# Kernel optimization log

Measured on AMD Instinct MI355X. Metric: run time of the kernel, lower is better.

The kernel has to match this reference:

```python
import jax, jax.numpy as jnp
import numpy as np

B, D, H, HD, L = 2, 768, 16, 48, 3
N_IMG, N_PAST, T_DEC = 1024, 16, 20

def _ln(x, g, b, eps=1e-5):
    m = jnp.mean(x, axis=-1, keepdims=True)
    v = jnp.mean(jnp.square(x - m), axis=-1, keepdims=True)
    return (x - m) * jax.lax.rsqrt(v + eps) * g + b

def _encoder(x, ln1_g, ln1_b, qkv_W, qkv_b, out_W, out_b, ln2_g, ln2_b, ff1_W, ff1_b, ff2_W, ff2_b):
    Bs, S, _ = x.shape
    keep = jnp.tril(jnp.ones((S, S), dtype=bool))  # causal: True = attend
    neg = jnp.asarray(jnp.finfo(x.dtype).min, x.dtype)
    scale = 1.0 / np.sqrt(HD)
    for l in range(L):  # pre-norm TransformerEncoderLayer, activation=relu (torch default)
        h = _ln(x, ln1_g[l], ln1_b[l])
        q, k, v = jnp.split(h @ qkv_W[l] + qkv_b[l], 3, axis=-1)
        q = q.reshape(Bs, S, H, HD); k = k.reshape(Bs, S, H, HD); v = v.reshape(Bs, S, H, HD)
        scores = jnp.einsum('bqhd,bkhd->bhqk', q, k) * scale
        attn = jax.nn.softmax(jnp.where(keep, scores, neg), axis=-1)
        ctx = jnp.einsum('bhqk,bkhd->bqhd', attn, v).reshape(Bs, S, H * HD)
        x = x + ctx @ out_W[l] + out_b[l]
        h = _ln(x, ln2_g[l], ln2_b[l])
        x = x + jax.nn.relu(h @ ff1_W[l] + ff1_b[l]) @ ff2_W[l] + ff2_b[l]
    return x

def setup_inputs():
    key = jax.random.key(0)
    ks = jax.random.split(key, 16)
    rn = lambda i, shp, s=0.02: jax.random.normal(ks[i], shp, jnp.float32) * s
    return {
        'feats': jax.random.normal(ks[0], (B, D, N_IMG), jnp.float32),
        'past': jax.random.normal(ks[1], (B, N_PAST, 6), jnp.float32),
        'intent': jax.random.randint(ks[2], (B,), 0, 3),
        'img_pos_enc': rn(3, (1, N_IMG, D)),
        'time_embeds': rn(4, (36, D)),
        'intent_embeds': rn(5, (3, D)),
        'past_W': rn(6, (6, D)), 'past_b': jnp.zeros((D,), jnp.float32),
        'pos_W': rn(7, (2, D)), 'pos_b': jnp.zeros((D,), jnp.float32),
        'ln1_g': jnp.ones((L, D), jnp.float32), 'ln1_b': jnp.zeros((L, D), jnp.float32),
        'qkv_W': rn(8, (L, D, 3 * D)), 'qkv_b': jnp.zeros((L, 3 * D), jnp.float32),
        'out_W': rn(9, (L, D, D)), 'out_b': jnp.zeros((L, D), jnp.float32),
        'ln2_g': jnp.ones((L, D), jnp.float32), 'ln2_b': jnp.zeros((L, D), jnp.float32),
        'ff1_W': rn(10, (L, D, 4 * D)), 'ff1_b': jnp.zeros((L, 4 * D), jnp.float32),
        'ff2_W': rn(11, (L, 4 * D, D)), 'ff2_b': jnp.zeros((L, D), jnp.float32),
        'dec1_W': rn(12, (D, D)), 'dec1_b': jnp.zeros((D,), jnp.float32),
        'dec2_W': rn(13, (D, 2)), 'dec2_b': jnp.zeros((2,), jnp.float32),
    }

def reference(feats, past, intent, img_pos_enc, time_embeds, intent_embeds,
              past_W, past_b, pos_W, pos_b,
              ln1_g, ln1_b, qkv_W, qkv_b, out_W, out_b, ln2_g, ln2_b,
              ff1_W, ff1_b, ff2_W, ff2_b, dec1_W, dec1_b, dec2_W, dec2_b):
    # context: 1024 image tokens + 1 intent token + 16 past tokens
    img_tokens = jnp.transpose(feats, (0, 2, 1)) + img_pos_enc          # [B, 1024, D]
    intent_idx = jnp.clip(intent - 1, 0, 2)
    intent_tok = intent_embeds[intent_idx][:, None, :]                  # [B, 1, D]
    past_toks = past @ past_W + past_b + time_embeds[:N_PAST]           # [B, 16, D]
    seq = jnp.concatenate([img_tokens, intent_tok, past_toks], axis=1)  # [B, 1041, D]
    enc = lambda s: _encoder(s, ln1_g, ln1_b, qkv_W, qkv_b, out_W, out_b,
                             ln2_g, ln2_b, ff1_W, ff1_b, ff2_W, ff2_b)
    preds = []
    for t in range(T_DEC):  # AR decode: full recompute each step, no KV cache (as in source)
        out = enc(seq)
        h = out[:, -1:, :]
        p = jax.nn.gelu(h @ dec1_W + dec1_b, approximate=False) @ dec2_W + dec2_b  # [B,1,2]
        preds.append(p)
        nxt = p @ pos_W + pos_b + time_embeds[N_PAST + t]
        seq = jnp.concatenate([seq, nxt], axis=1)
    return jnp.concatenate(preds, axis=1)  # [B, 20, 2]
```

## Files before the change

### kernel.cpp

```cpp
#include <hip/hip_runtime.h>
#include <math.h>

#define BB 2
#define DD 768
#define HH 16
#define HDIM 48
#define LL 3
#define NIMG 1024
#define NPAST 16
#define TDEC 20
#define SEQ0 1041
#define SPAD 1064
#define MM (BB*SEQ0)
#define SCALE_QK 0.14433756729740643f
#define KVL_C ((size_t)BB*HH*SPAD*HDIM)

typedef __attribute__((ext_vector_type(4))) float f32x4;
typedef __attribute__((ext_vector_type(8))) short bf16x8;

__device__ __forceinline__ short f2bf(float x) {
  unsigned u = __float_as_uint(x);
  unsigned r = (u + 0x7FFFu + ((u >> 16) & 1u)) >> 16;
  return (short)r;
}
__device__ __forceinline__ float bf2f(short h) {
  return __uint_as_float(((unsigned)(unsigned short)h) << 16);
}

__device__ __forceinline__ float block_sum256(float v, float* red) {
#pragma unroll
  for (int off = 32; off; off >>= 1) v += __shfl_down(v, off);
  __syncthreads();
  if ((threadIdx.x & 63) == 0) red[threadIdx.x >> 6] = v;
  __syncthreads();
  return red[0] + red[1] + red[2] + red[3];
}

__global__ __launch_bounds__(256) void build_img_kernel(
    const float* __restrict__ feats, const float* __restrict__ pe, float* __restrict__ x)
{
  __shared__ float T[64][65];
  int b = blockIdx.y;
  int s0 = blockIdx.x * 64;
  int tid = threadIdx.x;
  int r = tid >> 2;
  int c0 = (tid & 3) << 4;
  for (int d0 = 0; d0 < 768; d0 += 64) {
    const float* fp = feats + ((size_t)b*768 + d0 + r)*1024 + s0 + c0;
#pragma unroll
    for (int i = 0; i < 16; ++i) T[r][c0 + i] = fp[i];
    __syncthreads();
    float* xp = x + ((size_t)(b*SEQ0 + s0 + r))*768 + d0 + c0;
    const float* pp = pe + (size_t)(s0 + r)*768 + d0 + c0;
#pragma unroll
    for (int i = 0; i < 16; ++i) xp[i] = T[c0 + i][r] + pp[i];
    __syncthreads();
  }
}

__global__ __launch_bounds__(256) void build_misc_kernel(
    const float* __restrict__ past, const int* __restrict__ intent,
    const float* __restrict__ int_emb, const float* __restrict__ past_W,
    const float* __restrict__ past_b, const float* __restrict__ te,
    float* __restrict__ x)
{
  int b = blockIdx.y;
  int i = blockIdx.x;
  int tid = threadIdx.x;
  if (i == 0) {
    int idx = intent[b] - 1;
    idx = max(0, min(2, idx));
    for (int d = tid; d < 768; d += 256)
      x[((size_t)(b*SEQ0 + 1024))*768 + d] = int_emb[idx*768 + d];
  } else {
    int pi = i - 1;
    float p0 = past[(b*NPAST + pi)*6 + 0], p1 = past[(b*NPAST + pi)*6 + 1];
    float p2 = past[(b*NPAST + pi)*6 + 2], p3 = past[(b*NPAST + pi)*6 + 3];
    float p4 = past[(b*NPAST + pi)*6 + 4], p5 = past[(b*NPAST + pi)*6 + 5];
    for (int d = tid; d < 768; d += 256) {
      float s = past_b[d] + te[(size_t)pi*768 + d];
      s += p0*past_W[0*768 + d] + p1*past_W[1*768 + d] + p2*past_W[2*768 + d];
      s += p3*past_W[3*768 + d] + p4*past_W[4*768 + d] + p5*past_W[5*768 + d];
      x[((size_t)(b*SEQ0 + 1025 + pi))*768 + d] = s;
    }
  }
}

__global__ __launch_bounds__(256) void ln_kernel(
    const float* __restrict__ x, const float* __restrict__ g,
    const float* __restrict__ bta, float* __restrict__ h)
{
  __shared__ float red[4];
  size_t row = blockIdx.x;
  const float* xr = x + row*768;
  float* hr = h + row*768;
  int tid = threadIdx.x;
  float v0 = xr[tid], v1 = xr[tid+256], v2 = xr[tid+512];
  float m = block_sum256(v0+v1+v2, red) * (1.f/768.f);
  float d0 = v0-m, d1 = v1-m, d2 = v2-m;
  float var = block_sum256(d0*d0 + d1*d1 + d2*d2, red) * (1.f/768.f);
  float inv = rsqrtf(var + 1e-5f);
  hr[tid]     = d0*inv*g[tid]     + bta[tid];
  hr[tid+256] = d1*inv*g[tid+256] + bta[tid+256];
  hr[tid+512] = d2*inv*g[tid+512] + bta[tid+512];
}

__global__ __launch_bounds__(256) void wconv_kernel(
    const float* __restrict__ W, short* __restrict__ th, short* __restrict__ tl,
    int K, int N)
{
  __shared__ float T[64][68];
  int n0 = blockIdx.x * 64, k0 = blockIdx.y * 64;
  int t = threadIdx.x;
  int r = t >> 2, c0 = (t & 3) * 16;
  const float* src = W + (size_t)(k0 + r)*N + n0 + c0;
#pragma unroll
  for (int j = 0; j < 4; ++j) {
    f32x4 v = *(const f32x4*)(src + 4*j);
    T[r][c0 + 4*j + 0] = v.x; T[r][c0 + 4*j + 1] = v.y;
    T[r][c0 + 4*j + 2] = v.z; T[r][c0 + 4*j + 3] = v.w;
  }
  __syncthreads();
  bf16x8 h0, h1, l0, l1;
#pragma unroll
  for (int i = 0; i < 8; ++i) {
    float x = T[c0 + i][r];
    short hh = f2bf(x);
    h0[i] = hh; l0[i] = f2bf(x - bf2f(hh));
    float y = T[c0 + 8 + i][r];
    short hy = f2bf(y);
    h1[i] = hy; l1[i] = f2bf(y - bf2f(hy));
  }
  size_t dst = (size_t)(n0 + r)*K + k0 + c0;
  *(bf16x8*)(th + dst) = h0;
  *(bf16x8*)(th + dst + 8) = h1;
  *(bf16x8*)(tl + dst) = l0;
  *(bf16x8*)(tl + dst + 8) = l1;
}

__global__ __launch_bounds__(256) void gemm_mfma_kernel(
    const float* __restrict__ A, const short* __restrict__ Wh,
    const short* __restrict__ Wl, const float* __restrict__ bias,
    float* __restrict__ C, int M, int N, int K, int mode)
{
  __shared__ short As[2][128][40];
  __shared__ short Bs[2][128][40];
  int tid = threadIdx.x;
  int n0 = blockIdx.x * 128, m0 = blockIdx.y * 128;
  int wid = tid >> 6, l = tid & 63;
  int wm = wid >> 1, wn = wid & 1;
  int fr = l & 15, fk = (l >> 4) * 8;
  f32x4 acc[4][4] = {};
  int arow = tid >> 1, akh = (tid & 1) * 16;
  const float* aptr = A + (size_t)(m0 + arow)*K + akh;
  bool aval = (m0 + arow) < M;

  for (int k0 = 0; k0 < K; k0 += 32) {
    {
      float xv[16];
      if (aval) {
        const float* ap = aptr + k0;
#pragma unroll
        for (int j = 0; j < 4; ++j) {
          f32x4 v = *(const f32x4*)(ap + 4*j);
          xv[4*j+0] = v.x; xv[4*j+1] = v.y; xv[4*j+2] = v.z; xv[4*j+3] = v.w;
        }
      } else {
#pragma unroll
        for (int j = 0; j < 16; ++j) xv[j] = 0.f;
      }
      bf16x8 h0, h1, l0, l1;
#pragma unroll
      for (int e = 0; e < 8; ++e) {
        short hh = f2bf(xv[e]);
        h0[e] = hh; l0[e] = f2bf(xv[e] - bf2f(hh));
        short hy = f2bf(xv[8+e]);
        h1[e] = hy; l1[e] = f2bf(xv[8+e] - bf2f(hy));
      }
      *(bf16x8*)&As[0][arow][akh]     = h0;
      *(bf16x8*)&As[0][arow][akh + 8] = h1;
      *(bf16x8*)&As[1][arow][akh]     = l0;
      *(bf16x8*)&As[1][arow][akh + 8] = l1;
    }
#pragma unroll
    for (int cc = 0; cc < 2; ++cc) {
      int c = tid + cc*256;
      int row = c >> 2, woff = (c & 3) * 8;
      size_t src = (size_t)(n0 + row)*K + k0 + woff;
      *(bf16x8*)&Bs[0][row][woff] = *(const bf16x8*)(Wh + src);
      *(bf16x8*)&Bs[1][row][woff] = *(const bf16x8*)(Wl + src);
    }
    __syncthreads();
    bf16x8 af[4][2], bfv[4][2];
#pragma unroll
    for (int i = 0; i < 4; ++i) {
#pragma unroll
      for (int p = 0; p < 2; ++p) {
        af[i][p]  = *(const bf16x8*)&As[p][wm*64 + i*16 + fr][fk];
        bfv[i][p] = *(const bf16x8*)&Bs[p][wn*64 + i*16 + fr][fk];
      }
    }
#pragma unroll
    for (int im = 0; im < 4; ++im) {
#pragma unroll
      for (int in = 0; in < 4; ++in) {
        acc[im][in] = __builtin_amdgcn_mfma_f32_16x16x32_bf16(af[im][0], bfv[in][0], acc[im][in], 0, 0, 0);
        acc[im][in] = __builtin_amdgcn_mfma_f32_16x16x32_bf16(af[im][0], bfv[in][1], acc[im][in], 0, 0, 0);
        acc[im][in] = __builtin_amdgcn_mfma_f32_16x16x32_bf16(af[im][1], bfv[in][0], acc[im][in], 0, 0, 0);
      }
    }
    __syncthreads();
  }
#pragma unroll
  for (int in = 0; in < 4; ++in) {
    int n = n0 + wn*64 + in*16 + (l & 15);
    float bv = bias[n];
#pragma unroll
    for (int im = 0; im < 4; ++im) {
      f32x4 v = acc[im][in];
#pragma unroll
      for (int r = 0; r < 4; ++r) {
        int m = m0 + wm*64 + im*16 + (l >> 4)*4 + r;
        if (m < M) {
          float x = v[r] + bv;
          float* cp = &C[(size_t)m*N + n];
          if (mode == 1) x = fmaxf(x, 0.f);
          if (mode == 2) x += *cp;
          *cp = x;
        }
      }
    }
  }
}

__global__ __launch_bounds__(256) void scatter_kv_kernel(
    const float* __restrict__ qkv, float* __restrict__ kc, float* __restrict__ vc,
    int S, int spad)
{
  int s = blockIdx.x, b = blockIdx.y;
  const float* row = qkv + ((size_t)b*S + s)*2304;
  int tid = threadIdx.x;
#pragma unroll
  for (int i = 0; i < 3; ++i) {
    int j = tid + i*256;
    int hh = j / 48, hd = j - hh*48;
    size_t dst = ((size_t)(b*16 + hh)*spad + s)*48 + hd;
    kc[dst] = row[768 + j];
    vc[dst] = row[1536 + j];
  }
}

__global__ __launch_bounds__(256) void attn_prefill_kernel(
    const float* __restrict__ qkv, const float* __restrict__ Kc,
    const float* __restrict__ Vc, float* __restrict__ ctx, int S, int spad)
{
  __shared__ float Qs[32][49];
  __shared__ float Ks[64][49];
  __shared__ float Vs[64][49];
  __shared__ float Ps[32][65];
  __shared__ float mrow[32], lrow[32], resc[32];
  int tid = threadIdx.x;
  int qt = blockIdx.x, h = blockIdx.y, b = blockIdx.z;
  int q0 = qt * 32;
  for (int i = tid; i < 32*48; i += 256) {
    int r = i / 48, d = i - r*48;
    int s = q0 + r;
    Qs[r][d] = (s < S) ? qkv[((size_t)(b*S + s))*2304 + h*48 + d] * SCALE_QK : 0.f;
  }
  if (tid < 32) { mrow[tid] = -INFINITY; lrow[tid] = 0.f; }
  float acc[2][3] = {};
  int pr0 = (tid >> 4) << 1;
  int pc  = tid & 15;
  int sr  = tid & 31;
  int skg = tid >> 5;
  int q_last = min(q0 + 31, S - 1);
  const float* Kb = Kc + (size_t)(b*16 + h)*spad*48;
  const float* Vb = Vc + (size_t)(b*16 + h)*spad*48;
  __syncthreads();
  float qreg[48];
#pragma unroll
  for (int d = 0; d < 48; ++d) qreg[d] = Qs[sr][d];
  for (int k0 = 0; k0 <= q_last; k0 += 64) {
    int kn = min(64, q_last - k0 + 1);
    for (int i = tid; i < 64*48; i += 256) {
      int r = i / 48, d = i - r*48;
      bool ok = r < kn;
      Ks[r][d] = ok ? Kb[(size_t)(k0 + r)*48 + d] : 0.f;
      Vs[r][d] = ok ? Vb[(size_t)(k0 + r)*48 + d] : 0.f;
    }
    __syncthreads();
    {
      int qg = q0 + sr;
#pragma unroll
      for (int jj = 0; jj < 8; ++jj) {
        int k = skg*8 + jj;
        float s = 0.f;
#pragma unroll
        for (int d = 0; d < 48; ++d) s += qreg[d] * Ks[k][d];
        int kg = k0 + k;
        bool valid = (qg < S) && (k < kn) && (kg <= qg);
        Ps[sr][k] = valid ? s : -INFINITY;
      }
    }
    __syncthreads();
    {
      int r = tid >> 3;
      int c0 = (tid & 7) * 8;
      float mold = mrow[r];
      float mx = mold;
      float pv[8];
#pragma unroll
      for (int j = 0; j < 8; ++j) { pv[j] = Ps[r][c0 + j]; mx = fmaxf(mx, pv[j]); }
#pragma unroll
      for (int m = 1; m < 8; m <<= 1) mx = fmaxf(mx, __shfl_xor(mx, m));
      float psum = 0.f;
      if (mx > -INFINITY) {
#pragma unroll
        for (int j = 0; j < 8; ++j) {
          float p = __expf(pv[j] - mx);
          Ps[r][c0 + j] = p;
          psum += p;
        }
      } else {
#pragma unroll
        for (int j = 0; j < 8; ++j) Ps[r][c0 + j] = 0.f;
      }
#pragma unroll
      for (int m = 1; m < 8; m <<= 1) psum += __shfl_xor(psum, m);
      if ((tid & 7) == 0) {
        if (mx > -INFINITY) {
          float rs = (mold > -INFINITY) ? __expf(mold - mx) : 0.f;
          lrow[r] = lrow[r]*rs + psum;
          mrow[r] = mx;
          resc[r] = rs;
        } else {
          resc[r] = 1.f;
        }
      }
    }
    __syncthreads();
#pragma unroll
    for (int rr = 0; rr < 2; ++rr) {
      int r = pr0 + rr;
      float f = resc[r];
      float a0 = acc[rr][0]*f, a1 = acc[rr][1]*f, a2 = acc[rr][2]*f;
#pragma unroll 16
      for (int k = 0; k < 64; ++k) {
        float p = Ps[r][k];
        a0 += p * Vs[k][pc*3+0];
        a1 += p * Vs[k][pc*3+1];
        a2 += p * Vs[k][pc*3+2];
      }
      acc[rr][0] = a0; acc[rr][1] = a1; acc[rr][2] = a2;
    }
    __syncthreads();
  }
#pragma unroll
  for (int rr = 0; rr < 2; ++rr) {
    int r = pr0 + rr, s = q0 + r;
    if (s < S) {
      float invl = 1.f / lrow[r];
      float* cp = &ctx[((size_t)(b*S + s))*768 + h*48 + pc*3];
      cp[0] = acc[rr][0]*invl; cp[1] = acc[rr][1]*invl; cp[2] = acc[rr][2]*invl;
    }
  }
}

struct DecParams {
  const float *qkv_W, *qkv_b, *out_W, *out_b;
  const float *ln1_g, *ln1_b, *ln2_g, *ln2_b;
  const float *ff1_W, *ff1_b, *ff2_W, *ff2_b;
  const float *dec1_W, *dec1_b, *dec2_W, *dec2_b;
  const float *pos_W, *pos_b, *time_e;
  const float *xlast;
  float *Kc, *Vc;
  float *x_tok, *x_in_buf, *x_mid_buf;
  float *qkv_part, *out_part, *ff1_part, *ff2_part, *dec1_part;
  float *attn_m, *attn_l, *attn_o;
  float *outp;
};

__global__ __launch_bounds__(256) void k_qkvA(DecParams P, int l) {
  int p = blockIdx.x;
  __shared__ float xin[2][768];
  __shared__ float hn[2][768];
  __shared__ float part[4][2][64];
  __shared__ float red[4];
  int tid = threadIdx.x;
  if (l == 0) {
    for (int i = tid; i < 1536; i += 256) ((float*)xin)[i] = P.x_tok[i];
  } else {
    for (int i = tid; i < 1536; i += 256) {
      float v = P.x_mid_buf[i];
#pragma unroll
      for (int s = 0; s < 21; ++s) v += P.ff2_part[s*1536 + i];
      ((float*)xin)[i] = v;
    }
  }
  __syncthreads();
  if (p == 0) {
    for (int i = tid; i < 1536; i += 256) P.x_in_buf[i] = ((float*)xin)[i];
  }
  const float* g  = P.ln1_g + l*768;
  const float* be = P.ln1_b + l*768;
#pragma unroll
  for (int b = 0; b < 2; ++b) {
    float v0 = xin[b][tid], v1 = xin[b][tid+256], v2 = xin[b][tid+512];
    float m = block_sum256(v0+v1+v2, red) * (1.f/768.f);
    float d0=v0-m, d1=v1-m, d2=v2-m;
    float var = block_sum256(d0*d0+d1*d1+d2*d2, red) * (1.f/768.f);
    float inv = rsqrtf(var + 1e-5f);
    hn[b][tid]     = d0*inv*g[tid]     + be[tid];
    hn[b][tid+256] = d1*inv*g[tid+256] + be[tid+256];
    hn[b][tid+512] = d2*inv*g[tid+512] + be[tid+512];
  }
  __syncthreads();
  int nt = p % 36, ks = p / 36;
  int k0 = (ks*768)/7, k1 = ((ks+1)*768)/7;
  int w = tid >> 6, lane = tid & 63;
  int kw0 = k0 + ((k1-k0)*w)/4, kw1 = k0 + ((k1-k0)*(w+1))/4;
  int n = nt*64 + lane;
  const float* wp = P.qkv_W + (size_t)l*768*2304 + n;
  float a0 = 0.f, a1 = 0.f;
#pragma unroll 4
  for (int k = kw0; k < kw1; ++k) {
    float w_ = wp[(size_t)k*2304];
    a0 += hn[0][k]*w_; a1 += hn[1][k]*w_;
  }
  part[w][0][lane] = a0; part[w][1][lane] = a1;
  __syncthreads();
  if (tid < 128) {
    int b = tid>>6, ln = tid&63;
    float s = part[0][b][ln]+part[1][b][ln]+part[2][b][ln]+part[3][b][ln];
    P.qkv_part[ks*4608 + b*2304 + nt*64 + ln] = s;
  }
}

__global__ __launch_bounds__(256) void k_attn(DecParams P, int l, int pos) {
  __shared__ float qs[48], ksn[48], vsn[48];
  __shared__ float redm[4], reds[4];
  __shared__ float aw[4][48];
  int p = blockIdx.x;
  int b = p >> 7, h = (p >> 3) & 15, s = p & 7;
  int tid = threadIdx.x;
  const float* qb = P.qkv_b + l*2304;
  if (tid < 48) {
    float q  = qb[h*48+tid];
    float kk = qb[768 + h*48+tid];
    float vv = qb[1536 + h*48+tid];
#pragma unroll
    for (int ss = 0; ss < 7; ++ss) {
      const float* pp = P.qkv_part + ss*4608 + b*2304;
      q  += pp[h*48+tid];
      kk += pp[768 + h*48+tid];
      vv += pp[1536 + h*48+tid];
    }
    if (s == 7) {
      size_t coff = (size_t)l*KVL_C + ((size_t)(b*16+h)*SPAD + pos)*48 + tid;
      P.Kc[coff] = kk;
      P.Vc[coff] = vv;
    }
    qs[tid] = q * SCALE_QK; ksn[tid] = kk; vsn[tid] = vv;
  }
  __syncthreads();
  int CH = (pos + 7) >> 3;
  int r0 = s*CH, r1 = min(r0 + CH, pos);
  int nold = r1 - r0;
  bool is_new = (s == 7) && (tid == nold);
  bool active = (tid < nold) || is_new;
  const float* Kb = P.Kc + (size_t)l*KVL_C + (size_t)(b*16+h)*SPAD*48;
  const float* Vb = P.Vc + (size_t)l*KVL_C + (size_t)(b*16+h)*SPAD*48;
  float sc = -INFINITY;
  if (tid < nold) {
    const float4* kr = (const float4*)(Kb + (size_t)(r0+tid)*48);
    float ssum = 0.f;
#pragma unroll
    for (int i = 0; i < 12; ++i) {
      float4 kv = kr[i];
      ssum += qs[4*i]*kv.x + qs[4*i+1]*kv.y + qs[4*i+2]*kv.z + qs[4*i+3]*kv.w;
    }
    sc = ssum;
  } else if (is_new) {
    float ssum = 0.f;
#pragma unroll
    for (int d = 0; d < 48; ++d) ssum += qs[d]*ksn[d];
    sc = ssum;
  }
  float mx = sc;
#pragma unroll
  for (int o2 = 32; o2; o2 >>= 1) mx = fmaxf(mx, __shfl_down(mx, o2));
  if ((tid & 63) == 0) redm[tid >> 6] = mx;
  __syncthreads();
  float M = fmaxf(fmaxf(redm[0], redm[1]), fmaxf(redm[2], redm[3]));
  float pr = active ? __expf(sc - M) : 0.f;
  float lsum = block_sum256(pr, reds);
  float4 a[12];
  if (tid < nold) {
    const float4* vr = (const float4*)(Vb + (size_t)(r0+tid)*48);
#pragma unroll
    for (int i = 0; i < 12; ++i) {
      float4 vv = vr[i];
      a[i].x = pr*vv.x; a[i].y = pr*vv.y; a[i].z = pr*vv.z; a[i].w = pr*vv.w;
    }
  } else if (is_new) {
#pragma unroll
    for (int i = 0; i < 12; ++i) {
      a[i].x = pr*vsn[4*i]; a[i].y = pr*vsn[4*i+1];
      a[i].z = pr*vsn[4*i+2]; a[i].w = pr*vsn[4*i+3];
    }
  } else {
#pragma unroll
    for (int i = 0; i < 12; ++i) a[i] = make_float4(0.f,0.f,0.f,0.f);
  }
#pragma unroll
  for (int i = 0; i < 12; ++i) {
    float x0=a[i].x, x1=a[i].y, x2=a[i].z, x3=a[i].w;
#pragma unroll
    for (int o2 = 32; o2; o2 >>= 1) {
      x0 += __shfl_down(x0, o2); x1 += __shfl_down(x1, o2);
      x2 += __shfl_down(x2, o2); x3 += __shfl_down(x3, o2);
    }
    if ((tid & 63) == 0) {
      int w = tid >> 6;
      aw[w][4*i] = x0; aw[w][4*i+1] = x1; aw[w][4*i+2] = x2; aw[w][4*i+3] = x3;
    }
  }
  __syncthreads();
  int idx = (b*16 + h)*8 + s;
  if (tid == 0) { P.attn_m[idx] = M; P.attn_l[idx] = lsum; }
  if (tid < 48) P.attn_o[idx*48 + tid] = aw[0][tid]+aw[1][tid]+aw[2][tid]+aw[3][tid];
}

__global__ __launch_bounds__(256) void k_out(DecParams P, int l) {
  int p = blockIdx.x;
  __shared__ float ctx_s[2][96];
  __shared__ float opart[4][2][64][2];
  int nt = p / 8, ks = p % 8;
  int k0 = ks * 96;
  int tid = threadIdx.x;
  if (tid < 192) {
    int b = tid / 96, dl = tid % 96;
    int d = k0 + dl;
    int h = d / 48, dd = d % 48;
    int base = (b*16 + h)*8;
    float M = -INFINITY;
#pragma unroll
    for (int s2 = 0; s2 < 8; ++s2) M = fmaxf(M, P.attn_m[base+s2]);
    float L = 0.f, o = 0.f;
#pragma unroll
    for (int s2 = 0; s2 < 8; ++s2) {
      float e = __expf(P.attn_m[base+s2] - M);
      L += P.attn_l[base+s2]*e;
      o += P.attn_o[(base+s2)*48 + dd]*e;
    }
    ctx_s[b][dl] = o / L;
  }
  __syncthreads();
  int w = tid >> 6, lane = tid & 63;
  int n0 = nt * 128;
  const float* W = P.out_W + (size_t)l*768*768;
  float a00=0.f, a01=0.f, a10=0.f, a11=0.f;
#pragma unroll 4
  for (int j = w*24; j < w*24 + 24; ++j) {
    int kk = k0 + j;
    float2 wv = *(const float2*)&W[(size_t)kk*768 + n0 + lane*2];
    float c0 = ctx_s[0][j], c1 = ctx_s[1][j];
    a00 += c0*wv.x; a01 += c0*wv.y;
    a10 += c1*wv.x; a11 += c1*wv.y;
  }
  opart[w][0][lane][0] = a00; opart[w][0][lane][1] = a01;
  opart[w][1][lane][0] = a10; opart[w][1][lane][1] = a11;
  __syncthreads();
  {
    int b = tid >> 7, idx = tid & 127;
    int l2 = idx >> 1, c = idx & 1;
    float v = opart[0][b][l2][c] + opart[1][b][l2][c]
            + opart[2][b][l2][c] + opart[3][b][l2][c];
    P.out_part[ks*1536 + b*768 + n0 + idx] = v;
  }
}

__global__ __launch_bounds__(256) void k_ff1A(DecParams P, int l) {
  int p = blockIdx.x;
  __shared__ float xm[2][768];
  __shared__ float hn[2][768];
  __shared__ float part[4][2][64];
  __shared__ float red[4];
  int tid = threadIdx.x;
  const float* ob = P.out_b + l*768;
  for (int i = tid; i < 1536; i += 256) {
    int b = i / 768, d = i - b*768;
    float v = P.x_in_buf[i] + ob[d];
#pragma unroll
    for (int s = 0; s < 8; ++s) v += P.out_part[s*1536 + i];
    xm[b][d] = v;
  }
  __syncthreads();
  if (p == 0) {
    for (int i = tid; i < 1536; i += 256) P.x_mid_buf[i] = ((float*)xm)[i];
  }
  const float* g  = P.ln2_g + l*768;
  const float* be = P.ln2_b + l*768;
#pragma unroll
  for (int b = 0; b < 2; ++b) {
    float v0 = xm[b][tid], v1 = xm[b][tid+256], v2 = xm[b][tid+512];
    float m = block_sum256(v0+v1+v2, red) * (1.f/768.f);
    float d0=v0-m, d1=v1-m, d2=v2-m;
    float var = block_sum256(d0*d0+d1*d1+d2*d2, red) * (1.f/768.f);
    float inv = rsqrtf(var + 1e-5f);
    hn[b][tid]     = d0*inv*g[tid]     + be[tid];
    hn[b][tid+256] = d1*inv*g[tid+256] + be[tid+256];
    hn[b][tid+512] = d2*inv*g[tid+512] + be[tid+512];
  }
  __syncthreads();
  int nt = p % 48, ks = p / 48;
  int k0 = (ks*768)/5, k1 = ((ks+1)*768)/5;
  int w = tid >> 6, lane = tid & 63;
  int kw0 = k0 + ((k1-k0)*w)/4, kw1 = k0 + ((k1-k0)*(w+1))/4;
  int n = nt*64 + lane;
  const float* wp = P.ff1_W + (size_t)l*768*3072 + n;
  float a0 = 0.f, a1 = 0.f;
#pragma unroll 4
  for (int k = kw0; k < kw1; ++k) {
    float w_ = wp[(size_t)k*3072];
    a0 += hn[0][k]*w_; a1 += hn[1][k]*w_;
  }
  part[w][0][lane] = a0; part[w][1][lane] = a1;
  __syncthreads();
  if (tid < 128) {
    int b = tid>>6, ln = tid&63;
    float s = part[0][b][ln]+part[1][b][ln]+part[2][b][ln]+part[3][b][ln];
    P.ff1_part[ks*6144 + b*3072 + nt*64 + ln] = s;
  }
}

__global__ __launch_bounds__(256) void k_ff2A(DecParams P, int l) {
  int p = blockIdx.x;
  __shared__ float hseg[2][148];
  __shared__ float part[4][2][64];
  int tid = threadIdx.x;
  int nt = p % 12, ks = p / 12;
  int k0 = (ks*3072)/21, k1 = ((ks+1)*3072)/21;
  int kn = k1 - k0;
  const float* fb = P.ff1_b + l*3072;
  for (int i = tid; i < 2*kn; i += 256) {
    int b = i / kn, j = i - b*kn;
    float v = fb[k0+j];
#pragma unroll
    for (int s = 0; s < 5; ++s) v += P.ff1_part[s*6144 + b*3072 + k0 + j];
    hseg[b][j] = fmaxf(v, 0.f);
  }
  __syncthreads();
  int w = tid >> 6, lane = tid & 63;
  int jw0 = (kn*w)/4, jw1 = (kn*(w+1))/4;
  int n = nt*64 + lane;
  const float* wp = P.ff2_W + (size_t)l*3072*768 + n;
  float a0 = 0.f, a1 = 0.f;
#pragma unroll 4
  for (int j = jw0; j < jw1; ++j) {
    float w_ = wp[(size_t)(k0+j)*768];
    a0 += hseg[0][j]*w_; a1 += hseg[1][j]*w_;
  }
  part[w][0][lane] = a0; part[w][1][lane] = a1;
  __syncthreads();
  if (tid < 128) {
    int b = tid>>6, ln = tid&63;
    P.ff2_part[ks*1536 + b*768 + nt*64 + ln] =
        part[0][b][ln]+part[1][b][ln]+part[2][b][ln]+part[3][b][ln];
  }
}

__global__ __launch_bounds__(256) void k_dec1A(DecParams P, int t) {
  int p = blockIdx.x;
  __shared__ float hseg[2][40];
  __shared__ float part[4][2][64];
  int tid = threadIdx.x;
  int nt = p % 12, ks = p / 12;
  int k0 = (ks*768)/21, k1 = ((ks+1)*768)/21;
  int kn = k1 - k0;
  for (int i = tid; i < 2*kn; i += 256) {
    int b = i / kn, j = i - b*kn;
    float v;
    if (t == 0) {
      v = P.xlast[(size_t)b*SEQ0*768 + k0 + j];
    } else {
      v = P.x_mid_buf[b*768 + k0 + j];
#pragma unroll
      for (int s = 0; s < 21; ++s) v += P.ff2_part[s*1536 + b*768 + k0 + j];
    }
    hseg[b][j] = v;
  }
  __syncthreads();
  int w = tid >> 6, lane = tid & 63;
  int jw0 = (kn*w)/4, jw1 = (kn*(w+1))/4;
  int n = nt*64 + lane;
  const float* wp = P.dec1_W + n;
  float a0 = 0.f, a1 = 0.f;
#pragma unroll 4
  for (int j = jw0; j < jw1; ++j) {
    float w_ = wp[(size_t)(k0+j)*768];
    a0 += hseg[0][j]*w_; a1 += hseg[1][j]*w_;
  }
  part[w][0][lane] = a0; part[w][1][lane] = a1;
  __syncthreads();
  if (tid < 128) {
    int b = tid>>6, ln = tid&63;
    P.dec1_part[ks*1536 + b*768 + nt*64 + ln] =
        part[0][b][ln]+part[1][b][ln]+part[2][b][ln]+part[3][b][ln];
  }
}

__global__ __launch_bounds__(256) void k_head2(DecParams P, int t, int write_next) {
  __shared__ float hd[2][768];
  __shared__ float ps[2][2];
  int tid = threadIdx.x;
  for (int i = tid; i < 1536; i += 256) {
    int b = i / 768, d = i - b*768;
    float v = P.dec1_b[d];
#pragma unroll
    for (int s = 0; s < 21; ++s) v += P.dec1_part[s*1536 + i];
    hd[b][d] = 0.5f*v*(1.f + erff(v*0.70710678118654752f));
  }
  __syncthreads();
  int w = tid >> 6, lane = tid & 63;
  int b = w >> 1, j = w & 1;
  float partial = 0.f;
  for (int k = lane; k < 768; k += 64) partial += hd[b][k] * P.dec2_W[k*2 + j];
#pragma unroll
  for (int off = 32; off; off >>= 1) partial += __shfl_down(partial, off);
  if (lane == 0) {
    float v = partial + P.dec2_b[j];
    ps[b][j] = v;
    P.outp[(b*TDEC + t)*2 + j] = v;
  }
  __syncthreads();
  if (write_next) {
    for (int i = tid; i < 1536; i += 256) {
      int b2 = i / 768, d = i - b2*768;
      P.x_tok[i] = ps[b2][0]*P.pos_W[d] + ps[b2][1]*P.pos_W[768 + d]
                 + P.pos_b[d] + P.time_e[(size_t)(NPAST + t)*768 + d];
    }
  }
}

extern "C" void kernel_launch(void* const* d_in, const int* in_sizes, int n_in,
                              void* d_out, int out_size, void* d_ws, size_t ws_size,
                              hipStream_t stream) {
  (void)in_sizes; (void)n_in; (void)out_size; (void)ws_size;
  const float* feats   = (const float*)d_in[0];
  const float* past    = (const float*)d_in[1];
  const int*   intent  = (const int*)d_in[2];
  const float* img_pos = (const float*)d_in[3];
  const float* time_e  = (const float*)d_in[4];
  const float* int_emb = (const float*)d_in[5];
  const float* past_W  = (const float*)d_in[6];
  const float* past_b  = (const float*)d_in[7];
  const float* pos_W   = (const float*)d_in[8];
  const float* pos_b   = (const float*)d_in[9];
  const float* ln1_g   = (const float*)d_in[10];
  const float* ln1_b   = (const float*)d_in[11];
  const float* qkv_W   = (const float*)d_in[12];
  const float* qkv_b   = (const float*)d_in[13];
  const float* out_W   = (const float*)d_in[14];
  const float* out_b   = (const float*)d_in[15];
  const float* ln2_g   = (const float*)d_in[16];
  const float* ln2_b   = (const float*)d_in[17];
  const float* ff1_W   = (const float*)d_in[18];
  const float* ff1_b   = (const float*)d_in[19];
  const float* ff2_W   = (const float*)d_in[20];
  const float* ff2_b   = (const float*)d_in[21];
  const float* dec1_W  = (const float*)d_in[22];
  const float* dec1_b  = (const float*)d_in[23];
  const float* dec2_W  = (const float*)d_in[24];
  const float* dec2_b  = (const float*)d_in[25];
  float* outp = (float*)d_out;

  float* ws = (float*)d_ws;
  size_t off = 0;
  float* xbuf = ws + off;   off += (size_t)MM*DD;
  float* hbuf = ws + off;   off += (size_t)MM*DD;
  float* ctxbuf = hbuf;
  float* bigbuf = ws + off; off += (size_t)MM*3072;
  float* Kc = ws + off;     off += (size_t)LL*BB*HH*SPAD*HDIM;
  float* Vc = ws + off;     off += (size_t)LL*BB*HH*SPAD*HDIM;
  float* x_tok = ws + off;    off += BB*DD;
  float* x_in_buf = ws + off; off += BB*DD;
  float* x_mid_buf = ws + off; off += BB*DD;
  float* qkv_part = ws + off;  off += 7*2*2304;
  float* out_part = ws + off;  off += 8*2*768;
  float* ff1_part = ws + off;  off += 5*2*3072;
  float* ff2_part = ws + off;  off += 21*2*768;
  float* dec1_part = ws + off; off += 21*2*768;
  float* attn_m = ws + off;    off += 2*16*8;
  float* attn_l = ws + off;    off += 2*16*8;
  float* attn_o = ws + off;    off += 2*16*8*48;
  short* wt_h = (short*)(ws + off); off += (size_t)768*3072/2;
  short* wt_l = (short*)(ws + off); off += (size_t)768*3072/2;

  const size_t KVL = (size_t)BB*HH*SPAD*HDIM;

  build_img_kernel<<<dim3(NIMG/64, BB), 256, 0, stream>>>(feats, img_pos, xbuf);
  build_misc_kernel<<<dim3(17, BB), 256, 0, stream>>>(past, intent, int_emb, past_W, past_b, time_e, xbuf);

  const int mtiles = (MM + 127) / 128;
  for (int l = 0; l < LL; ++l) {
    float* kcl = Kc + (size_t)l*KVL;
    float* vcl = Vc + (size_t)l*KVL;

    ln_kernel<<<MM, 256, 0, stream>>>(xbuf, ln1_g + l*DD, ln1_b + l*DD, hbuf);
    wconv_kernel<<<dim3(2304/64, 768/64), 256, 0, stream>>>(
        qkv_W + (size_t)l*DD*2304, wt_h, wt_l, DD, 2304);
    gemm_mfma_kernel<<<dim3(2304/128, mtiles), 256, 0, stream>>>(
        hbuf, wt_h, wt_l, qkv_b + l*2304, bigbuf, MM, 2304, DD, 0);

    scatter_kv_kernel<<<dim3(SEQ0, BB), 256, 0, stream>>>(bigbuf, kcl, vcl, SEQ0, SPAD);
    attn_prefill_kernel<<<dim3((SEQ0 + 31)/32, HH, BB), 256, 0, stream>>>(
        bigbuf, kcl, vcl, ctxbuf, SEQ0, SPAD);

    wconv_kernel<<<dim3(768/64, 768/64), 256, 0, stream>>>(
        out_W + (size_t)l*DD*DD, wt_h, wt_l, DD, 768);
    gemm_mfma_kernel<<<dim3(768/128, mtiles), 256, 0, stream>>>(
        ctxbuf, wt_h, wt_l, out_b + l*DD, xbuf, MM, 768, DD, 2);

    ln_kernel<<<MM, 256, 0, stream>>>(xbuf, ln2_g + l*DD, ln2_b + l*DD, hbuf);
    wconv_kernel<<<dim3(3072/64, 768/64), 256, 0, stream>>>(
        ff1_W + (size_t)l*DD*3072, wt_h, wt_l, DD, 3072);
    gemm_mfma_kernel<<<dim3(3072/128, mtiles), 256, 0, stream>>>(
        hbuf, wt_h, wt_l, ff1_b + l*3072, bigbuf, MM, 3072, DD, 1);

    wconv_kernel<<<dim3(768/64, 3072/64), 256, 0, stream>>>(
        ff2_W + (size_t)l*3072*DD, wt_h, wt_l, 3072, 768);
    gemm_mfma_kernel<<<dim3(768/128, mtiles), 256, 0, stream>>>(
        bigbuf, wt_h, wt_l, ff2_b + l*DD, xbuf, MM, 768, 3072, 2);
  }

  DecParams P;
  P.qkv_W = qkv_W; P.qkv_b = qkv_b; P.out_W = out_W; P.out_b = out_b;
  P.ln1_g = ln1_g; P.ln1_b = ln1_b; P.ln2_g = ln2_g; P.ln2_b = ln2_b;
  P.ff1_W = ff1_W; P.ff1_b = ff1_b; P.ff2_W = ff2_W; P.ff2_b = ff2_b;
  P.dec1_W = dec1_W; P.dec1_b = dec1_b; P.dec2_W = dec2_W; P.dec2_b = dec2_b;
  P.pos_W = pos_W; P.pos_b = pos_b; P.time_e = time_e;
  P.xlast = xbuf + (size_t)(SEQ0 - 1)*DD;
  P.Kc = Kc; P.Vc = Vc;
  P.x_tok = x_tok; P.x_in_buf = x_in_buf; P.x_mid_buf = x_mid_buf;
  P.qkv_part = qkv_part; P.out_part = out_part; P.ff1_part = ff1_part;
  P.ff2_part = ff2_part; P.dec1_part = dec1_part;
  P.attn_m = attn_m; P.attn_l = attn_l; P.attn_o = attn_o;
  P.outp = outp;

  k_dec1A<<<252, 256, 0, stream>>>(P, 0);
  k_head2<<<1, 256, 0, stream>>>(P, 0, 1);
  for (int t = 1; t < TDEC; ++t) {
    int pos = SEQ0 + t - 1;
    for (int l = 0; l < LL; ++l) {
      k_qkvA<<<252, 256, 0, stream>>>(P, l);
      k_attn<<<256, 256, 0, stream>>>(P, l, pos);
      k_out<<<48, 256, 0, stream>>>(P, l);
      k_ff1A<<<240, 256, 0, stream>>>(P, l);
      k_ff2A<<<252, 256, 0, stream>>>(P, l);
    }
    k_dec1A<<<252, 256, 0, stream>>>(P, t);
    k_head2<<<1, 256, 0, stream>>>(P, t, (t < TDEC - 1) ? 1 : 0);
  }
}
```

Measured before the change: 4.975 ms.

## Emit split-bf16 activations from producers and fuse KV scatter into QKV GEMM

Producer kernels (layernorm, attention output, FF1 GEMM epilogue) now write activations directly as hi/lo bf16 pairs, so the GEMM loads bf16 tiles instead of converting fp32 inputs every k-step. The standalone scatter_kv kernel is removed and the QKV GEMM epilogue writes K and V straight into the cache layout. This cuts redundant conversion work (each A tile was re-split once per N-tile block) and one kernel launch with its memory pass. The cost is scattered, uncoalesced stores in the QKV epilogue.

```diff
diff --git a/kernel.cpp b/kernel.cpp
--- a/kernel.cpp
+++ b/kernel.cpp
@@ -86,23 +86,27 @@
   }
 }
 
-__global__ __launch_bounds__(256) void ln_kernel(
+__global__ __launch_bounds__(256) void ln_bf_kernel(
     const float* __restrict__ x, const float* __restrict__ g,
-    const float* __restrict__ bta, float* __restrict__ h)
+    const float* __restrict__ bta, short* __restrict__ hh, short* __restrict__ hl)
 {
   __shared__ float red[4];
   size_t row = blockIdx.x;
   const float* xr = x + row*768;
-  float* hr = h + row*768;
   int tid = threadIdx.x;
   float v0 = xr[tid], v1 = xr[tid+256], v2 = xr[tid+512];
   float m = block_sum256(v0+v1+v2, red) * (1.f/768.f);
   float d0 = v0-m, d1 = v1-m, d2 = v2-m;
   float var = block_sum256(d0*d0 + d1*d1 + d2*d2, red) * (1.f/768.f);
   float inv = rsqrtf(var + 1e-5f);
-  hr[tid]     = d0*inv*g[tid]     + bta[tid];
-  hr[tid+256] = d1*inv*g[tid+256] + bta[tid+256];
-  hr[tid+512] = d2*inv*g[tid+512] + bta[tid+512];
+  float o0 = d0*inv*g[tid]     + bta[tid];
+  float o1 = d1*inv*g[tid+256] + bta[tid+256];
+  float o2 = d2*inv*g[tid+512] + bta[tid+512];
+  short h0 = f2bf(o0), h1 = f2bf(o1), h2 = f2bf(o2);
+  size_t base = row*768;
+  hh[base+tid]     = h0; hl[base+tid]     = f2bf(o0 - bf2f(h0));
+  hh[base+tid+256] = h1; hl[base+tid+256] = f2bf(o1 - bf2f(h1));
+  hh[base+tid+512] = h2; hl[base+tid+512] = f2bf(o2 - bf2f(h2));
 }
 
 __global__ __launch_bounds__(256) void wconv_kernel(
@@ -138,10 +142,13 @@
   *(bf16x8*)(tl + dst + 8) = l1;
 }
 
-__global__ __launch_bounds__(256) void gemm_mfma_kernel(
-    const float* __restrict__ A, const short* __restrict__ Wh,
-    const short* __restrict__ Wl, const float* __restrict__ bias,
-    float* __restrict__ C, int M, int N, int K, int mode)
+__global__ __launch_bounds__(256) void gemm_bf_kernel(
+    const short* __restrict__ Ah, const short* __restrict__ Al,
+    const short* __restrict__ Wh, const short* __restrict__ Wl,
+    const float* __restrict__ bias, float* __restrict__ C,
+    short* __restrict__ Ch, short* __restrict__ Cl,
+    int M, int N, int K, int mode,
+    float* __restrict__ kc, float* __restrict__ vc)
 {
   __shared__ short As[2][128][40];
   __shared__ short Bs[2][128][40];
@@ -152,35 +159,20 @@
   int fr = l & 15, fk = (l >> 4) * 8;
   f32x4 acc[4][4] = {};
   int arow = tid >> 1, akh = (tid & 1) * 16;
-  const float* aptr = A + (size_t)(m0 + arow)*K + akh;
   bool aval = (m0 + arow) < M;
+  size_t abase = (size_t)(m0 + arow)*K + akh;
 
   for (int k0 = 0; k0 < K; k0 += 32) {
-    {
-      float xv[16];
-      if (aval) {
-        const float* ap = aptr + k0;
-#pragma unroll
-        for (int j = 0; j < 4; ++j) {
-          f32x4 v = *(const f32x4*)(ap + 4*j);
-          xv[4*j+0] = v.x; xv[4*j+1] = v.y; xv[4*j+2] = v.z; xv[4*j+3] = v.w;
-        }
-      } else {
-#pragma unroll
-        for (int j = 0; j < 16; ++j) xv[j] = 0.f;
-      }
-      bf16x8 h0, h1, l0, l1;
-#pragma unroll
-      for (int e = 0; e < 8; ++e) {
-        short hh = f2bf(xv[e]);
-        h0[e] = hh; l0[e] = f2bf(xv[e] - bf2f(hh));
-        short hy = f2bf(xv[8+e]);
-        h1[e] = hy; l1[e] = f2bf(xv[8+e] - bf2f(hy));
-      }
-      *(bf16x8*)&As[0][arow][akh]     = h0;
-      *(bf16x8*)&As[0][arow][akh + 8] = h1;
-      *(bf16x8*)&As[1][arow][akh]     = l0;
-      *(bf16x8*)&As[1][arow][akh + 8] = l1;
+    if (aval) {
+      size_t src = abase + k0;
+      *(bf16x8*)&As[0][arow][akh]     = *(const bf16x8*)(Ah + src);
+      *(bf16x8*)&As[0][arow][akh + 8] = *(const bf16x8*)(Ah + src + 8);
+      *(bf16x8*)&As[1][arow][akh]     = *(const bf16x8*)(Al + src);
+      *(bf16x8*)&As[1][arow][akh + 8] = *(const bf16x8*)(Al + src + 8);
+    } else {
+      bf16x8 z = {};
+      *(bf16x8*)&As[0][arow][akh] = z; *(bf16x8*)&As[0][arow][akh + 8] = z;
+      *(bf16x8*)&As[1][arow][akh] = z; *(bf16x8*)&As[1][arow][akh + 8] = z;
     }
 #pragma unroll
     for (int cc = 0; cc < 2; ++cc) {
@@ -223,36 +215,37 @@
         int m = m0 + wm*64 + im*16 + (l >> 4)*4 + r;
         if (m < M) {
           float x = v[r] + bv;
-          float* cp = &C[(size_t)m*N + n];
-          if (mode == 1) x = fmaxf(x, 0.f);
-          if (mode == 2) x += *cp;
-          *cp = x;
+          size_t off = (size_t)m*N + n;
+          if (mode == 1) {
+            x = fmaxf(x, 0.f);
+            short hh = f2bf(x);
+            Ch[off] = hh;
+            Cl[off] = f2bf(x - bf2f(hh));
+          } else if (mode == 2) {
+            C[off] += x;
+          } else {
+            C[off] = x;
+            if (mode == 3 && n >= 768) {
+              int b = m / SEQ0, s = m - b*SEQ0;
+              int j = n - 768;
+              if (j < 768)
+                kc[((size_t)(b*16 + j/48)*SPAD + s)*48 + (j % 48)] = x;
+              else {
+                j -= 768;
+                vc[((size_t)(b*16 + j/48)*SPAD + s)*48 + (j % 48)] = x;
+              }
+            }
+          }
         }
       }
     }
   }
 }
 
-__global__ __launch_bounds__(256) void scatter_kv_kernel(
-    const float* __restrict__ qkv, float* __restrict__ kc, float* __restrict__ vc,
-    int S, int spad)
-{
-  int s = blockIdx.x, b = blockIdx.y;
-  const float* row = qkv + ((size_t)b*S + s)*2304;
-  int tid = threadIdx.x;
-#pragma unroll
-  for (int i = 0; i < 3; ++i) {
-    int j = tid + i*256;
-    int hh = j / 48, hd = j - hh*48;
-    size_t dst = ((size_t)(b*16 + hh)*spad + s)*48 + hd;
-    kc[dst] = row[768 + j];
-    vc[dst] = row[1536 + j];
-  }
-}
-
 __global__ __launch_bounds__(256) void attn_prefill_kernel(
     const float* __restrict__ qkv, const float* __restrict__ Kc,
-    const float* __restrict__ Vc, float* __restrict__ ctx, int S, int spad)
+    const float* __restrict__ Vc, short* __restrict__ ctxh, short* __restrict__ ctxl,
+    int S, int spad)
 {
   __shared__ float Qs[32][49];
   __shared__ float Ks[64][49];
@@ -360,8 +353,14 @@
     int r = pr0 + rr, s = q0 + r;
     if (s < S) {
       float invl = 1.f / lrow[r];
-      float* cp = &ctx[((size_t)(b*S + s))*768 + h*48 + pc*3];
-      cp[0] = acc[rr][0]*invl; cp[1] = acc[rr][1]*invl; cp[2] = acc[rr][2]*invl;
+      size_t off = ((size_t)(b*S + s))*768 + h*48 + pc*3;
+#pragma unroll
+      for (int j = 0; j < 3; ++j) {
+        float val = acc[rr][j]*invl;
+        short hh = f2bf(val);
+        ctxh[off + j] = hh;
+        ctxl[off + j] = f2bf(val - bf2f(hh));
+      }
     }
   }
 }
@@ -778,9 +777,11 @@
   float* ws = (float*)d_ws;
   size_t off = 0;
   float* xbuf = ws + off;   off += (size_t)MM*DD;
-  float* hbuf = ws + off;   off += (size_t)MM*DD;
-  float* ctxbuf = hbuf;
+  short* hh = (short*)(ws + off); off += (size_t)MM*DD/2;
+  short* hl = (short*)(ws + off); off += (size_t)MM*DD/2;
   float* bigbuf = ws + off; off += (size_t)MM*3072;
+  short* bigh = (short*)bigbuf;
+  short* bigl = bigh + (size_t)MM*3072;
   float* Kc = ws + off;     off += (size_t)LL*BB*HH*SPAD*HDIM;
   float* Vc = ws + off;     off += (size_t)LL*BB*HH*SPAD*HDIM;
   float* x_tok = ws + off;    off += BB*DD;
@@ -807,31 +808,34 @@
     float* kcl = Kc + (size_t)l*KVL;
     float* vcl = Vc + (size_t)l*KVL;
 
-    ln_kernel<<<MM, 256, 0, stream>>>(xbuf, ln1_g + l*DD, ln1_b + l*DD, hbuf);
+    ln_bf_kernel<<<MM, 256, 0, stream>>>(xbuf, ln1_g + l*DD, ln1_b + l*DD, hh, hl);
     wconv_kernel<<<dim3(2304/64, 768/64), 256, 0, stream>>>(
         qkv_W + (size_t)l*DD*2304, wt_h, wt_l, DD, 2304);
-    gemm_mfma_kernel<<<dim3(2304/128, mtiles), 256, 0, stream>>>(
-        hbuf, wt_h, wt_l, qkv_b + l*2304, bigbuf, MM, 2304, DD, 0);
-
-    scatter_kv_kernel<<<dim3(SEQ0, BB), 256, 0, stream>>>(bigbuf, kcl, vcl, SEQ0, SPAD);
+    gemm_bf_kernel<<<dim3(2304/128, mtiles), 256, 0, stream>>>(
+        hh, hl, wt_h, wt_l, qkv_b + l*2304, bigbuf, nullptr, nullptr,
+        MM, 2304, DD, 3, kcl, vcl);
+
     attn_prefill_kernel<<<dim3((SEQ0 + 31)/32, HH, BB), 256, 0, stream>>>(
-        bigbuf, kcl, vcl, ctxbuf, SEQ0, SPAD);
+        bigbuf, kcl, vcl, hh, hl, SEQ0, SPAD);
 
     wconv_kernel<<<dim3(768/64, 768/64), 256, 0, stream>>>(
         out_W + (size_t)l*DD*DD, wt_h, wt_l, DD, 768);
-    gemm_mfma_kernel<<<dim3(768/128, mtiles), 256, 0, stream>>>(
-        ctxbuf, wt_h, wt_l, out_b + l*DD, xbuf, MM, 768, DD, 2);
-
-    ln_kernel<<<MM, 256, 0, stream>>>(xbuf, ln2_g + l*DD, ln2_b + l*DD, hbuf);
+    gemm_bf_kernel<<<dim3(768/128, mtiles), 256, 0, stream>>>(
+        hh, hl, wt_h, wt_l, out_b + l*DD, xbuf, nullptr, nullptr,
+        MM, 768, DD, 2, nullptr, nullptr);
+
+    ln_bf_kernel<<<MM, 256, 0, stream>>>(xbuf, ln2_g + l*DD, ln2_b + l*DD, hh, hl);
     wconv_kernel<<<dim3(3072/64, 768/64), 256, 0, stream>>>(
         ff1_W + (size_t)l*DD*3072, wt_h, wt_l, DD, 3072);
-    gemm_mfma_kernel<<<dim3(3072/128, mtiles), 256, 0, stream>>>(
-        hbuf, wt_h, wt_l, ff1_b + l*3072, bigbuf, MM, 3072, DD, 1);
+    gemm_bf_kernel<<<dim3(3072/128, mtiles), 256, 0, stream>>>(
+        hh, hl, wt_h, wt_l, ff1_b + l*3072, nullptr, bigh, bigl,
+        MM, 3072, DD, 1, nullptr, nullptr);
 
     wconv_kernel<<<dim3(768/64, 3072/64), 256, 0, stream>>>(
         ff2_W + (size_t)l*3072*DD, wt_h, wt_l, 3072, 768);
-    gemm_mfma_kernel<<<dim3(768/128, mtiles), 256, 0, stream>>>(
-        bigbuf, wt_h, wt_l, ff2_b + l*DD, xbuf, MM, 768, 3072, 2);
+    gemm_bf_kernel<<<dim3(768/128, mtiles), 256, 0, stream>>>(
+        bigh, bigl, wt_h, wt_l, ff2_b + l*DD, xbuf, nullptr, nullptr,
+        MM, 768, 3072, 2, nullptr, nullptr);
   }
 
   DecParams P;
```

Result: faster. 4.831 ms, median of 2 (-2.9%).
